# Kernel optimization log

Measured on AMD Instinct MI355X. Metric: run time of the kernel, lower is better.

## Reference

```python
import jax, jax.numpy as jnp
import numpy as np

N = 100_000          # NEURON_COUNT (scaled)
INPUT_SIZE = 1024    # input neurons occupy indices [0, INPUT_SIZE)
OUTPUT_SIZE = 256    # output neurons occupy indices [N-OUTPUT_SIZE, N)
E = 10_000_000       # SYNAPSE_RATIO * N
STEPS = 3


def setup_inputs() -> dict:
    key = jax.random.key(0)
    k1, k2, k3, k4, k5 = jax.random.split(key, 5)
    x = jax.random.normal(k1, (INPUT_SIZE,), dtype=jnp.float32)
    synapse_weights = jax.random.normal(k2, (E,), dtype=jnp.float32)
    neuron_biases = jax.random.normal(k3, (N - INPUT_SIZE,), dtype=jnp.float32)
    synapse_src = jax.random.randint(k4, (E,), 0, N, dtype=jnp.int64) if jax.config.jax_enable_x64 else jax.random.randint(k4, (E,), 0, N, dtype=jnp.int32)
    synapse_dst = jax.random.randint(k5, (E,), 0, N, dtype=jnp.int64) if jax.config.jax_enable_x64 else jax.random.randint(k5, (E,), 0, N, dtype=jnp.int32)
    return {
        "x": x,
        "synapse_weights": synapse_weights,
        "neuron_biases": neuron_biases,
        "synapse_src": synapse_src,
        "synapse_dst": synapse_dst,
    }


def reference(x, synapse_weights, neuron_biases, synapse_src, synapse_dst):
    # Initial state: zeros everywhere, inputs injected at the first INPUT_SIZE slots.
    v = jnp.zeros((N,), dtype=x.dtype).at[:INPUT_SIZE].set(x.reshape(-1))
    # tanh applied to all neurons except outputs (last OUTPUT_SIZE indices)
    tanh_mask = jnp.arange(N) < (N - OUTPUT_SIZE)
    for _ in range(STEPS):
        # vectorized gather-multiply-scatter: next[to] += v[from] * w  (one segment_sum)
        msg = v[synapse_src] * synapse_weights                       # [E]
        nxt = jax.ops.segment_sum(msg, synapse_dst, num_segments=N)  # [N]
        # biases added to all non-input neurons
        nxt = nxt.at[INPUT_SIZE:].add(neuron_biases)
        # tanh everywhere except output neurons
        v = jnp.where(tanh_mask, jnp.tanh(nxt), nxt)
    return v[N - OUTPUT_SIZE:]
```

## Files before the change

### kernel.cpp

```cpp
#include <hip/hip_runtime.h>

#define N_NEURONS   100000
#define INPUT_SIZE  1024
#define OUTPUT_SIZE 256
#define E_SYN       10000000
#define STEPS       3

#define RANGES      16
#define BIN         6250
#define SHIFT       13
#define DMASK       8191
#define SCAT_BLK    512
#define CBLK        64
#define RG          8
#define RSL         (CBLK / RG)
#define CAP         665600
#define VEC4        (E_SYN / 4)

#define CHK         1024
#define NCH         9766
#define PITER       (CHK / 256)
#define PW          4
#define HIST_GRID   ((NCH + PW - 1) / PW)
#define SCJ         ((NCH + 1023) / 1024)

#define CMB(x, b0, b1, b2, b3) \
    ((((x) & 1) ? (b0) : ~(b0)) & (((x) & 2) ? (b1) : ~(b1)) & \
     (((x) & 4) ? (b2) : ~(b2)) & (((x) & 8) ? (b3) : ~(b3)))

__global__ __launch_bounds__(256) void hist_kernel(const float* __restrict__ x,
                                                   float* __restrict__ v,
                                                   const int* __restrict__ dst,
                                                   int* __restrict__ hist) {
    const int gidx = blockIdx.x * 256 + threadIdx.x;
    if (gidx < N_NEURONS) v[gidx] = (gidx < INPUT_SIZE) ? x[gidx] : 0.0f;
    const int lane  = threadIdx.x & 63;
    const int wv    = threadIdx.x >> 6;
    const int chunk = blockIdx.x * PW + wv;
    if (chunk >= NCH) return;
    const int beg = chunk * CHK;
    const int4* dst4 = (const int4*)dst;
    int h = 0;
    for (int it = 0; it < PITER; ++it) {
        int e   = beg + (it * 64 + lane) * 4;
        bool ok = (e < E_SYN);
        int4 d4 = ok ? dst4[e >> 2] : make_int4(0, 0, 0, 0);
        unsigned long long okm = __ballot(ok);
        int rk[4] = {d4.x / BIN, d4.y / BIN, d4.z / BIN, d4.w / BIN};
#pragma unroll
        for (int k = 0; k < 4; ++k) {
            unsigned long long b0 = __ballot(rk[k] & 1);
            unsigned long long b1 = __ballot(rk[k] & 2);
            unsigned long long b2 = __ballot(rk[k] & 4);
            unsigned long long b3 = __ballot(rk[k] & 8);
            h += __popcll(CMB(lane, b0, b1, b2, b3) & okm);
        }
    }
    if (lane < RANGES) hist[(size_t)lane * NCH + chunk] = h;
}

__global__ __launch_bounds__(1024) void scan_kernel(const int* __restrict__ hist,
                                                    int* __restrict__ bases,
                                                    int* __restrict__ gcur) {
    const int r = blockIdx.x;
    const int t = threadIdx.x;
    const int lane = t & 63;
    const int wv   = t >> 6;
    int vals[SCJ];
    int s = 0;
#pragma unroll
    for (int j = 0; j < SCJ; ++j) {
        int idx = t * SCJ + j;
        int vv  = (idx < NCH) ? hist[(size_t)r * NCH + idx] : 0;
        vals[j] = vv;
        s += vv;
    }
    int x = s;
#pragma unroll
    for (int d = 1; d < 64; d <<= 1) {
        int y = __shfl_up(x, d, 64);
        if (lane >= d) x += y;
    }
    __shared__ int wsum[16];
    if (lane == 63) wsum[wv] = x;
    __syncthreads();
    if (wv == 0) {
        int y = (lane < 16) ? wsum[lane] : 0;
        int z = y;
#pragma unroll
        for (int d = 1; d < 16; d <<= 1) {
            int u = __shfl_up(z, d, 64);
            if (lane >= d) z += u;
        }
        if (lane < 16) wsum[lane] = z - y;
    }
    __syncthreads();
    int run = (x - s) + wsum[wv];
#pragma unroll
    for (int j = 0; j < SCJ; ++j) {
        int idx = t * SCJ + j;
        if (idx < NCH) bases[(size_t)r * NCH + idx] = r * CAP + run;
        run += vals[j];
    }
    if (t == 1023) gcur[r] = run;
}

__global__ __launch_bounds__(256) void partition_kernel(
        const float* __restrict__ w,
        const int*   __restrict__ src,
        const int*   __restrict__ dst,
        const int*   __restrict__ bases,
        int2* __restrict__ recs) {
    const int lane  = threadIdx.x & 63;
    const int wv    = threadIdx.x >> 6;
    const int chunk = blockIdx.x * PW + wv;
    if (chunk >= NCH) return;
    const unsigned long long ltmask = (1ull << lane) - 1ull;

    int cur = 0;
    if (lane < RANGES) cur = bases[(size_t)lane * NCH + chunk];

    const int beg = chunk * CHK;
    const int4* dst4 = (const int4*)dst;
    const int4* src4 = (const int4*)src;
    const int4* wq4  = (const int4*)w;

    for (int it = 0; it < PITER; ++it) {
        int e   = beg + (it * 64 + lane) * 4;
        bool ok = (e < E_SYN);
        int idx = e >> 2;
        int4 d4 = ok ? dst4[idx] : make_int4(0, 0, 0, 0);
        int4 s4 = ok ? src4[idx] : make_int4(0, 0, 0, 0);
        int4 q4 = ok ? wq4[idx]  : make_int4(0, 0, 0, 0);
        unsigned long long okm = __ballot(ok);
        int dd[4] = {d4.x, d4.y, d4.z, d4.w};
        int ss[4] = {s4.x, s4.y, s4.z, s4.w};
        int qq[4] = {q4.x, q4.y, q4.z, q4.w};
#pragma unroll
        for (int k = 0; k < 4; ++k) {
            int d = dd[k];
            int r = d / BIN;
            unsigned long long b0 = __ballot(r & 1);
            unsigned long long b1 = __ballot(r & 2);
            unsigned long long b2 = __ballot(r & 4);
            unsigned long long b3 = __ballot(r & 8);
            unsigned long long mym = CMB(r, b0, b1, b2, b3) & okm;
            int rank = __popcll(mym & ltmask);
            int gpos = __shfl(cur, r, 64) + rank;
            if (ok) recs[(size_t)gpos] =
                make_int2((ss[k] << SHIFT) | (d - r * BIN), qq[k]);
            unsigned long long mm = CMB(lane, b0, b1, b2, b3) & okm;
            cur += __popcll(mm);
        }
    }
}

__global__ __launch_bounds__(SCAT_BLK) void scatter_sorted(
        const int2* __restrict__ recs,
        const int*  __restrict__ gcur,
        const float* __restrict__ v,
        float* __restrict__ partials) {
    __shared__ float bins[BIN];
    const int r = blockIdx.x / CBLK;
    const int c = blockIdx.x % CBLK;
    const int tid = threadIdx.x;
    for (int j = tid; j < BIN; j += SCAT_BLK) bins[j] = 0.0f;
    __syncthreads();

    const int cnt   = gcur[r];
    const int npair = cnt >> 1;
    const int4* base4 = (const int4*)(recs + (size_t)r * CAP);
    const int stride = CBLK * SCAT_BLK;
    int u = c * SCAT_BLK + tid;
    for (; u + 3 * stride < npair; u += 4 * stride) {
        int4 A[4];
#pragma unroll
        for (int i = 0; i < 4; ++i) A[i] = base4[u + i * stride];
        float g[8];
#pragma unroll
        for (int i = 0; i < 4; ++i) {
            g[2 * i]     = v[A[i].x >> SHIFT];
            g[2 * i + 1] = v[A[i].z >> SHIFT];
        }
#pragma unroll
        for (int i = 0; i < 4; ++i) {
            atomicAdd(&bins[A[i].x & DMASK], g[2 * i]     * __int_as_float(A[i].y));
            atomicAdd(&bins[A[i].z & DMASK], g[2 * i + 1] * __int_as_float(A[i].w));
        }
    }
    for (; u < npair; u += stride) {
        int4 a = base4[u];
        float v0 = v[a.x >> SHIFT];
        float v1 = v[a.z >> SHIFT];
        atomicAdd(&bins[a.x & DMASK], v0 * __int_as_float(a.y));
        atomicAdd(&bins[a.z & DMASK], v1 * __int_as_float(a.w));
    }
    if ((cnt & 1) && c == 0 && tid == 0) {
        int2 p = recs[(size_t)r * CAP + cnt - 1];
        atomicAdd(&bins[p.x & DMASK], v[p.x >> SHIFT] * __int_as_float(p.y));
    }
    __syncthreads();
    float* o = partials + (size_t)c * N_NEURONS + r * BIN;
    for (int j = tid; j < BIN; j += SCAT_BLK) o[j] = bins[j];
}

__global__ void reduce_fused(const float* __restrict__ partials,
                             const float* __restrict__ bias,
                             float* __restrict__ v,
                             float* __restrict__ out,
                             int write_out) {
    int i4 = 4 * (blockIdx.x * blockDim.x + threadIdx.x);
    if (i4 >= N_NEURONS) return;
    const float* base = partials + i4;
    float4 tot = {0.f, 0.f, 0.f, 0.f};
#pragma unroll 2
    for (int g = 0; g < RG; ++g) {
        float4 a = {0.f, 0.f, 0.f, 0.f};
#pragma unroll
        for (int cc = 0; cc < RSL; ++cc) {
            float4 p = *(const float4*)(base + (size_t)(g * RSL + cc) * N_NEURONS);
            a.x += p.x; a.y += p.y; a.z += p.z; a.w += p.w;
        }
        tot.x += a.x; tot.y += a.y; tot.z += a.z; tot.w += a.w;
    }
    float av[4] = {tot.x, tot.y, tot.z, tot.w};
#pragma unroll
    for (int k = 0; k < 4; ++k) {
        int i = i4 + k;
        float val = av[k] + ((i >= INPUT_SIZE) ? bias[i - INPUT_SIZE] : 0.0f);
        float nv  = (i < N_NEURONS - OUTPUT_SIZE) ? tanhf(val) : val;
        v[i] = nv;
        if (write_out && i >= N_NEURONS - OUTPUT_SIZE)
            out[i - (N_NEURONS - OUTPUT_SIZE)] = val;
    }
}

__global__ void init_state_fb(const float* __restrict__ x, float* __restrict__ v) {
    int i = blockIdx.x * blockDim.x + threadIdx.x;
    if (i < N_NEURONS) v[i] = (i < INPUT_SIZE) ? x[i] : 0.0f;
}
__global__ void scatter_binned(const float* __restrict__ w,
                               const int*   __restrict__ src,
                               const int*   __restrict__ dst,
                               const float* __restrict__ v,
                               float*       __restrict__ partials,
                               int C) {
    __shared__ float bins[BIN];
    const int r = blockIdx.x / C;
    const int c = blockIdx.x % C;
    const int lo = r * BIN;
    const int hi = lo + BIN;
    for (int j = threadIdx.x; j < BIN; j += blockDim.x) bins[j] = 0.0f;
    __syncthreads();
    const int4*   src4 = (const int4*)src;
    const int4*   dst4 = (const int4*)dst;
    const float4* w4v  = (const float4*)w;
    const int stride = C * blockDim.x;
    for (int u = c * blockDim.x + threadIdx.x; u < VEC4; u += stride) {
        const int4   s4 = src4[u];
        const int4   d4 = dst4[u];
        const float4 wv = w4v[u];
        int   s[4] = {s4.x, s4.y, s4.z, s4.w};
        int   d[4] = {d4.x, d4.y, d4.z, d4.w};
        float ww[4] = {wv.x, wv.y, wv.z, wv.w};
#pragma unroll
        for (int k = 0; k < 4; ++k)
            if (d[k] >= lo && d[k] < hi)
                atomicAdd(&bins[d[k] - lo], v[s[k]] * ww[k]);
    }
    __syncthreads();
    float* o = partials + (size_t)c * N_NEURONS + r * BIN;
    for (int j = threadIdx.x; j < BIN; j += blockDim.x) o[j] = bins[j];
}
__global__ void reduce_update_fb(const float* __restrict__ partials,
                                 const float* __restrict__ bias,
                                 float* __restrict__ v,
                                 float* __restrict__ out,
                                 int C, int write_out) {
    int i4 = 4 * (blockIdx.x * blockDim.x + threadIdx.x);
    if (i4 >= N_NEURONS) return;
    const float* base = partials + i4;
    float4 acc = {0.f, 0.f, 0.f, 0.f};
    for (int c = 0; c < C; ++c) {
        float4 p = *(const float4*)(base + (size_t)c * N_NEURONS);
        acc.x += p.x; acc.y += p.y; acc.z += p.z; acc.w += p.w;
    }
    float av[4] = {acc.x, acc.y, acc.z, acc.w};
#pragma unroll
    for (int k = 0; k < 4; ++k) {
        int i = i4 + k;
        float val = av[k] + ((i >= INPUT_SIZE) ? bias[i - INPUT_SIZE] : 0.0f);
        float nv  = (i < N_NEURONS - OUTPUT_SIZE) ? tanhf(val) : val;
        v[i] = nv;
        if (write_out && i >= N_NEURONS - OUTPUT_SIZE)
            out[i - (N_NEURONS - OUTPUT_SIZE)] = val;
    }
}

extern "C" void kernel_launch(void* const* d_in, const int* in_sizes, int n_in,
                              void* d_out, int out_size, void* d_ws, size_t ws_size,
                              hipStream_t stream) {
    const float* x    = (const float*)d_in[0];
    const float* w    = (const float*)d_in[1];
    const float* bias = (const float*)d_in[2];
    const int*   src  = (const int*)d_in[3];
    const int*   dst  = (const int*)d_in[4];
    float* out = (float*)d_out;

    const int blk = 256;
    const int grid_n   = (N_NEURONS + blk - 1) / blk;
    const int red_grid = (N_NEURONS / 4 + blk - 1) / blk;

    float* v        = (float*)d_ws;
    float* partials = v + N_NEURONS;
    int*   hist     = (int*)(partials + (size_t)CBLK * N_NEURONS);
    int*   bases    = hist + (size_t)RANGES * NCH;
    int*   gcur     = bases + (size_t)RANGES * NCH;
    int2*  recs     = (int2*)(gcur + RANGES);
    size_t need = (size_t)((char*)(recs + (size_t)RANGES * CAP) - (char*)d_ws);

    if (ws_size >= need) {
        hist_kernel<<<HIST_GRID, 256, 0, stream>>>(x, v, dst, hist);
        scan_kernel<<<RANGES, 1024, 0, stream>>>(hist, bases, gcur);
        partition_kernel<<<HIST_GRID, 256, 0, stream>>>(w, src, dst, bases, recs);
        for (int s = 0; s < STEPS; ++s) {
            scatter_sorted<<<RANGES * CBLK, SCAT_BLK, 0, stream>>>(
                recs, gcur, v, partials);
            reduce_fused<<<red_grid, blk, 0, stream>>>(
                partials, bias, v, out, s == STEPS - 1 ? 1 : 0);
        }
    } else {
        long C = (long)(ws_size / 4 / N_NEURONS) - 1;
        if (C > 64) C = 64;
        if (C < 1) C = 1;
        float* part_fb = v + N_NEURONS;
        init_state_fb<<<grid_n, blk, 0, stream>>>(x, v);
        for (int s = 0; s < STEPS; ++s) {
            scatter_binned<<<RANGES * (int)C, SCAT_BLK, 0, stream>>>(
                w, src, dst, v, part_fb, (int)C);
            reduce_update_fb<<<red_grid, blk, 0, stream>>>(
                part_fb, bias, v, out, (int)C, s == STEPS - 1 ? 1 : 0);
        }
    }
}
```

Baseline: 397.7 us.

## Add second-level partition by source range and gather from LDS-staged state

Adds a second partition pass that splits each destination-range record list into 16 source sub-ranges (histogram, scan, compose, scatter into a new records buffer). The per-step scatter kernel then stages the matching slice of the state vector in shared memory and gathers from LDS instead of doing random global loads. Partial sums drop from 64 to 16 slices per neuron, which shrinks the reduce pass. The cost is an extra one-time partition over all edges, twice the record workspace, and only 256 blocks of 1024 threads per step, which may limit parallelism and cause imbalance across categories.

```diff
diff --git a/kernel.cpp b/kernel.cpp
--- a/kernel.cpp
+++ b/kernel.cpp
@@ -10,10 +10,9 @@
 #define BIN         6250
 #define SHIFT       13
 #define DMASK       8191
-#define SCAT_BLK    512
-#define CBLK        64
-#define RG          8
-#define RSL         (CBLK / RG)
+#define NSB         16
+#define SBW         6250
+#define NCAT        (RANGES * NSB)
 #define CAP         665600
 #define VEC4        (E_SYN / 4)
 
@@ -23,6 +22,16 @@
 #define PW          4
 #define HIST_GRID   ((NCH + PW - 1) / PW)
 #define SCJ         ((NCH + 1023) / 1024)
+
+#define RCHK        1024
+#define JB          (CAP / RCHK)
+#define NCHB        (RANGES * JB)
+#define HB_GRID     ((NCHB + 3) / 4)
+#define SBJ         11
+
+#define SC_BLK      1024
+#define RG          4
+#define RSL         (NSB / RG)
 
 #define CMB(x, b0, b1, b2, b3) \
     ((((x) & 1) ? (b0) : ~(b0)) & (((x) & 2) ? (b1) : ~(b1)) & \
@@ -155,53 +164,207 @@
     }
 }
 
-__global__ __launch_bounds__(SCAT_BLK) void scatter_sorted(
-        const int2* __restrict__ recs,
-        const int*  __restrict__ gcur,
+__global__ __launch_bounds__(256) void histB_kernel(const int2* __restrict__ recs,
+                                                    const int*  __restrict__ gcur,
+                                                    int* __restrict__ histB) {
+    const int lane = threadIdx.x & 63;
+    const int wv   = threadIdx.x >> 6;
+    const int gid  = blockIdx.x * 4 + wv;
+    if (gid >= NCHB) return;
+    const int r = gid / JB;
+    const int j = gid - r * JB;
+    const int cnt = gcur[r];
+    int h = 0;
+    const int c = lane & 15;
+    if (j * RCHK < cnt) {
+        const int2* rb = recs + (size_t)r * CAP + (size_t)j * RCHK;
+        int lim = cnt - j * RCHK;
+        if (lim > RCHK) lim = RCHK;
+        for (int it = 0; it < RCHK / 64; ++it) {
+            int idx = it * 64 + lane;
+            bool ok = idx < lim;
+            int rx  = ok ? rb[idx].x : 0;
+            int sb  = (rx >> SHIFT) / SBW;
+            unsigned long long okm = __ballot(ok);
+            unsigned long long b0 = __ballot(sb & 1);
+            unsigned long long b1 = __ballot(sb & 2);
+            unsigned long long b2 = __ballot(sb & 4);
+            unsigned long long b3 = __ballot(sb & 8);
+            h += __popcll(CMB(c, b0, b1, b2, b3) & okm);
+        }
+    }
+    if (lane < NSB) histB[(size_t)(r * NSB + lane) * JB + j] = h;
+}
+
+__global__ __launch_bounds__(64) void scanB_kernel(const int* __restrict__ histB,
+                                                   int* __restrict__ basesB,
+                                                   int* __restrict__ totB) {
+    const int cat  = blockIdx.x;
+    const int lane = threadIdx.x;
+    int vals[SBJ];
+    int s = 0;
+#pragma unroll
+    for (int j = 0; j < SBJ; ++j) {
+        int idx = lane * SBJ + j;
+        int vv  = (idx < JB) ? histB[(size_t)cat * JB + idx] : 0;
+        vals[j] = vv;
+        s += vv;
+    }
+    int x = s;
+#pragma unroll
+    for (int d = 1; d < 64; d <<= 1) {
+        int y = __shfl_up(x, d, 64);
+        if (lane >= d) x += y;
+    }
+    int run = x - s;
+#pragma unroll
+    for (int j = 0; j < SBJ; ++j) {
+        int idx = lane * SBJ + j;
+        if (idx < JB) basesB[(size_t)cat * JB + idx] = run;
+        run += vals[j];
+    }
+    if (lane == 63) totB[cat] = x;
+}
+
+__global__ void composeB_kernel(const int* __restrict__ totB,
+                                int* __restrict__ catStart,
+                                int2* __restrict__ recs2) {
+    __shared__ int cs[NCAT];
+    const int t = threadIdx.x;
+    if (t < RANGES) {
+        int s = t * CAP;
+        for (int sb = 0; sb < NSB; ++sb) {
+            int c = t * NSB + sb;
+            cs[c] = s;
+            s = (s + totB[c] + 1) & ~1;
+        }
+    }
+    __syncthreads();
+    if (t < NCAT) {
+        catStart[t] = cs[t];
+        int tot = totB[t];
+        if (tot & 1) {
+            int sb = t & (NSB - 1);
+            recs2[(size_t)cs[t] + tot] = make_int2((sb * SBW) << SHIFT, 0);
+        }
+    }
+}
+
+__global__ __launch_bounds__(256) void partB_kernel(const int2* __restrict__ recs,
+                                                    const int*  __restrict__ gcur,
+                                                    const int*  __restrict__ histB,
+                                                    const int*  __restrict__ basesB,
+                                                    const int*  __restrict__ catStart,
+                                                    int2* __restrict__ recs2) {
+    __shared__ int2 tile[4][RCHK];
+    const int lane = threadIdx.x & 63;
+    const int wv   = threadIdx.x >> 6;
+    const int gid  = blockIdx.x * 4 + wv;
+    if (gid >= NCHB) return;
+    const int r = gid / JB;
+    const int j = gid - r * JB;
+    const int cnt = gcur[r];
+    if (j * RCHK >= cnt) return;
+    const unsigned long long ltmask = (1ull << lane) - 1ull;
+
+    int h = 0, gd = 0;
+    if (lane < NSB) {
+        h  = histB[(size_t)(r * NSB + lane) * JB + j];
+        gd = catStart[r * NSB + lane] + basesB[(size_t)(r * NSB + lane) * JB + j];
+    }
+    int x = h;
+#pragma unroll
+    for (int d = 1; d < 16; d <<= 1) {
+        int y = __shfl_up(x, d, 64);
+        if (lane >= d) x += y;
+    }
+    const int lb = x - h;
+
+    int2* tl = tile[wv];
+    const int4* rb4 = (const int4*)(recs + (size_t)r * CAP + (size_t)j * RCHK);
+    int lim = cnt - j * RCHK;
+    if (lim > RCHK) lim = RCHK;
+    int cnt_c = 0;
+    for (int it = 0; it < RCHK / 128; ++it) {
+        int pi = it * 64 + lane;
+        int4 p = rb4[pi];
+#pragma unroll
+        for (int k = 0; k < 2; ++k) {
+            bool ok = (pi * 2 + k) < lim;
+            int rx = ok ? (k ? p.z : p.x) : 0;
+            int ry = k ? p.w : p.y;
+            int sb = (rx >> SHIFT) / SBW;
+            unsigned long long okm = __ballot(ok);
+            unsigned long long b0 = __ballot(sb & 1);
+            unsigned long long b1 = __ballot(sb & 2);
+            unsigned long long b2 = __ballot(sb & 4);
+            unsigned long long b3 = __ballot(sb & 8);
+            unsigned long long mym = CMB(sb, b0, b1, b2, b3) & okm;
+            int rank = __popcll(mym & ltmask);
+            int pos  = __shfl(lb + cnt_c, sb, 64) + rank;
+            if (ok) tl[pos] = make_int2(rx, ry);
+            unsigned long long mm = CMB(lane, b0, b1, b2, b3) & okm;
+            cnt_c += __popcll(mm);
+        }
+    }
+    for (int c = 0; c < NSB; ++c) {
+        const int len = __shfl(cnt_c, c, 64);
+        const int lbc = __shfl(lb, c, 64);
+        const int gdc = __shfl(gd, c, 64);
+        for (int off = lane; off < len; off += 64)
+            recs2[(size_t)gdc + off] = tl[lbc + off];
+    }
+}
+
+__global__ __launch_bounds__(SC_BLK) void scatter_cat(
+        const int2* __restrict__ recs2,
+        const int*  __restrict__ catStart,
+        const int*  __restrict__ totB,
         const float* __restrict__ v,
         float* __restrict__ partials) {
     __shared__ float bins[BIN];
-    const int r = blockIdx.x / CBLK;
-    const int c = blockIdx.x % CBLK;
+    __shared__ float vst[SBW];
+    const int r   = blockIdx.x >> 4;
+    const int sb  = blockIdx.x & 15;
     const int tid = threadIdx.x;
-    for (int j = tid; j < BIN; j += SCAT_BLK) bins[j] = 0.0f;
-    __syncthreads();
-
-    const int cnt   = gcur[r];
-    const int npair = cnt >> 1;
-    const int4* base4 = (const int4*)(recs + (size_t)r * CAP);
-    const int stride = CBLK * SCAT_BLK;
-    int u = c * SCAT_BLK + tid;
-    for (; u + 3 * stride < npair; u += 4 * stride) {
-        int4 A[4];
-#pragma unroll
-        for (int i = 0; i < 4; ++i) A[i] = base4[u + i * stride];
-        float g[8];
-#pragma unroll
-        for (int i = 0; i < 4; ++i) {
-            g[2 * i]     = v[A[i].x >> SHIFT];
-            g[2 * i + 1] = v[A[i].z >> SHIFT];
-        }
-#pragma unroll
-        for (int i = 0; i < 4; ++i) {
+    for (int j = tid; j < BIN; j += SC_BLK) bins[j] = 0.0f;
+    const float2* vs2 = (const float2*)(v + sb * SBW);
+    float2* vt2 = (float2*)vst;
+    for (int j = tid; j < SBW / 2; j += SC_BLK) vt2[j] = vs2[j];
+    __syncthreads();
+
+    const int cat   = r * NSB + sb;
+    const int start = catStart[cat];
+    const int P     = (totB[cat] + 1) >> 1;
+    const int4* c4  = (const int4*)(recs2 + (size_t)start);
+    const int sbb   = sb * SBW;
+    int u = tid;
+    for (; u + 7 * SC_BLK < P; u += 8 * SC_BLK) {
+        int4 A[8];
+#pragma unroll
+        for (int i = 0; i < 8; ++i) A[i] = c4[u + i * SC_BLK];
+        float g[16];
+#pragma unroll
+        for (int i = 0; i < 8; ++i) {
+            g[2 * i]     = vst[(A[i].x >> SHIFT) - sbb];
+            g[2 * i + 1] = vst[(A[i].z >> SHIFT) - sbb];
+        }
+#pragma unroll
+        for (int i = 0; i < 8; ++i) {
             atomicAdd(&bins[A[i].x & DMASK], g[2 * i]     * __int_as_float(A[i].y));
             atomicAdd(&bins[A[i].z & DMASK], g[2 * i + 1] * __int_as_float(A[i].w));
         }
     }
-    for (; u < npair; u += stride) {
-        int4 a = base4[u];
-        float v0 = v[a.x >> SHIFT];
-        float v1 = v[a.z >> SHIFT];
+    for (; u < P; u += SC_BLK) {
+        int4 a = c4[u];
+        float v0 = vst[(a.x >> SHIFT) - sbb];
+        float v1 = vst[(a.z >> SHIFT) - sbb];
         atomicAdd(&bins[a.x & DMASK], v0 * __int_as_float(a.y));
         atomicAdd(&bins[a.z & DMASK], v1 * __int_as_float(a.w));
     }
-    if ((cnt & 1) && c == 0 && tid == 0) {
-        int2 p = recs[(size_t)r * CAP + cnt - 1];
-        atomicAdd(&bins[p.x & DMASK], v[p.x >> SHIFT] * __int_as_float(p.y));
-    }
-    __syncthreads();
-    float* o = partials + (size_t)c * N_NEURONS + r * BIN;
-    for (int j = tid; j < BIN; j += SCAT_BLK) o[j] = bins[j];
+    __syncthreads();
+    float* o = partials + (size_t)sb * N_NEURONS + r * BIN;
+    for (int j = tid; j < BIN; j += SC_BLK) o[j] = bins[j];
 }
 
 __global__ void reduce_fused(const float* __restrict__ partials,
@@ -213,7 +376,7 @@
     if (i4 >= N_NEURONS) return;
     const float* base = partials + i4;
     float4 tot = {0.f, 0.f, 0.f, 0.f};
-#pragma unroll 2
+#pragma unroll
     for (int g = 0; g < RG; ++g) {
         float4 a = {0.f, 0.f, 0.f, 0.f};
 #pragma unroll
@@ -313,30 +476,40 @@
 
     float* v        = (float*)d_ws;
     float* partials = v + N_NEURONS;
-    int*   hist     = (int*)(partials + (size_t)CBLK * N_NEURONS);
-    int*   bases    = hist + (size_t)RANGES * NCH;
-    int*   gcur     = bases + (size_t)RANGES * NCH;
+    int*   histA    = (int*)(partials + (size_t)NSB * N_NEURONS);
+    int*   basesA   = histA + (size_t)RANGES * NCH;
+    int*   histB    = basesA + (size_t)RANGES * NCH;
+    int*   basesB   = histB + (size_t)NCAT * JB;
+    int*   totB     = basesB + (size_t)NCAT * JB;
+    int*   catStart = totB + NCAT;
+    int*   gcur     = catStart + NCAT;
     int2*  recs     = (int2*)(gcur + RANGES);
-    size_t need = (size_t)((char*)(recs + (size_t)RANGES * CAP) - (char*)d_ws);
+    int2*  recs2    = recs + (size_t)RANGES * CAP;
+    size_t need = (size_t)((char*)(recs2 + (size_t)RANGES * CAP) - (char*)d_ws);
 
     if (ws_size >= need) {
-        hist_kernel<<<HIST_GRID, 256, 0, stream>>>(x, v, dst, hist);
-        scan_kernel<<<RANGES, 1024, 0, stream>>>(hist, bases, gcur);
-        partition_kernel<<<HIST_GRID, 256, 0, stream>>>(w, src, dst, bases, recs);
+        hist_kernel<<<HIST_GRID, 256, 0, stream>>>(x, v, dst, histA);
+        scan_kernel<<<RANGES, 1024, 0, stream>>>(histA, basesA, gcur);
+        partition_kernel<<<HIST_GRID, 256, 0, stream>>>(w, src, dst, basesA, recs);
+        histB_kernel<<<HB_GRID, 256, 0, stream>>>(recs, gcur, histB);
+        scanB_kernel<<<NCAT, 64, 0, stream>>>(histB, basesB, totB);
+        composeB_kernel<<<1, 256, 0, stream>>>(totB, catStart, recs2);
+        partB_kernel<<<HB_GRID, 256, 0, stream>>>(recs, gcur, histB, basesB,
+                                                  catStart, recs2);
         for (int s = 0; s < STEPS; ++s) {
-            scatter_sorted<<<RANGES * CBLK, SCAT_BLK, 0, stream>>>(
-                recs, gcur, v, partials);
+            scatter_cat<<<NCAT, SC_BLK, 0, stream>>>(
+                recs2, catStart, totB, v, partials);
             reduce_fused<<<red_grid, blk, 0, stream>>>(
                 partials, bias, v, out, s == STEPS - 1 ? 1 : 0);
         }
     } else {
         long C = (long)(ws_size / 4 / N_NEURONS) - 1;
-        if (C > 64) C = 64;
+        if (C > 16) C = 16;
         if (C < 1) C = 1;
         float* part_fb = v + N_NEURONS;
         init_state_fb<<<grid_n, blk, 0, stream>>>(x, v);
         for (int s = 0; s < STEPS; ++s) {
-            scatter_binned<<<RANGES * (int)C, SCAT_BLK, 0, stream>>>(
+            scatter_binned<<<RANGES * (int)C, SC_BLK, 0, stream>>>(
                 w, src, dst, v, part_fb, (int)C);
             reduce_update_fb<<<red_grid, blk, 0, stream>>>(
                 part_fb, bias, v, out, (int)C, s == STEPS - 1 ? 1 : 0);
```

Result: slower. 448.6 us (+12.8%).
